# Optimization experiments

Measured on AMD Instinct MI355X. Metric: run time of the kernel, lower is better.

Reference implementation:

```python
import jax, jax.numpy as jnp
import numpy as np

N, D, K = 131072, 256, 16      # samples, ambient dim, projection dims
NDOM, B, G = 8, 32, 100        # domains, hist_bins, barycenter grid size


def setup_inputs() -> dict:
    key = jax.random.key(0)
    k1, k2, k3, k4, k5, k6 = jax.random.split(key, 6)
    X = jax.random.normal(k1, (N, D), jnp.float32)
    y = jax.random.randint(k2, (N,), 0, NDOM)
    # wT: orthonormal columns via QR with sign fix (as in INB.__init__)
    wi = np.asarray(jax.random.normal(k3, (D, K), jnp.float32))
    Q, R = np.linalg.qr(wi)
    wT = jnp.asarray(Q * np.sign(np.diag(R)), jnp.float32)
    # Per-(domain, dim) histogram bin edges (sorted -> monotone) and CDF values in [0,1]
    bin_edges = jnp.sort(jax.random.normal(k4, (NDOM, K, B + 1), jnp.float32) * 2.0, axis=-1)
    steps = jax.random.uniform(k5, (NDOM, K, B), jnp.float32, minval=0.1, maxval=1.0)
    c = jnp.cumsum(steps, axis=-1)
    cdf_vals = jnp.concatenate([jnp.zeros((NDOM, K, 1), jnp.float32), c / c[..., -1:]], axis=-1)
    # Barycenter inverse-CDF (quantile function) sampled on a uniform grid over [0,1]
    bary_q = jnp.sort(jax.random.normal(k6, (K, G), jnp.float32) * 2.0, axis=-1)
    return {"X": X, "y": y, "wT": wT, "bin_edges": bin_edges,
            "cdf_vals": cdf_vals, "bary_q": bary_q}


def _searchsorted_2d(edges, x):
    # edges: (N, K, B+1) per-sample monotone edges; x: (N, K)
    ss = jax.vmap(jax.vmap(lambda e, v: jnp.searchsorted(e, v, side='right')))(edges, x)
    return jnp.clip(ss - 1, 0, B - 1)  # (N, K) int, left bin index


def reference(X, y, wT, bin_edges, cdf_vals, bary_q):
    Xm = X @ wT                         # (N, K) small-K GEMM
    remaining = X - Xm @ wT.T           # (N, D)
    # gather per-sample domain tables (irregular, data-dependent access)
    eb = bin_edges[y]                   # (N, K, B+1)
    cb = cdf_vals[y]                    # (N, K, B+1)
    i = _searchsorted_2d(eb, Xm)        # (N, K)
    x0 = jnp.take_along_axis(eb, i[..., None], axis=-1)[..., 0]
    x1 = jnp.take_along_axis(eb, i[..., None] + 1, axis=-1)[..., 0]
    f0 = jnp.take_along_axis(cb, i[..., None], axis=-1)[..., 0]
    f1 = jnp.take_along_axis(cb, i[..., None] + 1, axis=-1)[..., 0]
    t = jnp.clip((Xm - x0) / (x1 - x0), 0.0, 1.0)
    u = f0 + t * (f1 - f0)              # per-domain CDF value in [0,1]
    # barycenter inverse CDF: linear interp on uniform grid over [0,1]
    pos = jnp.clip(u, 0.0, 1.0) * (G - 1)
    j = jnp.clip(pos.astype(jnp.int32), 0, G - 2)
    tt = pos - j.astype(pos.dtype)
    kk = jnp.arange(K)[None, :]
    z = bary_q[kk, j] * (1.0 - tt) + bary_q[kk, j + 1] * tt  # (N, K)
    return remaining + z @ wT.T
```

## Files before the change

### kernel.cpp

```cpp
#include <hip/hip_runtime.h>

typedef float v2f __attribute__((ext_vector_type(2)));
typedef float v4f __attribute__((ext_vector_type(4)));

#define N_ROWS 131072
#define DIM    256
#define KP     16
#define NDOM   8
#define NB     32
#define GG     100

#define EB_N   (NDOM*KP*(NB+1))
#define BARY_N (KP*GG)

#define GRID   2048
#define WAVES  4
#define NWAVE  (GRID*WAVES)
#define PAIRS  8

__device__ __forceinline__ v2f swap32_sum(v2f lo, v2f hi, int lane) {
    bool up = (lane & 32) != 0;
    v2f keep = up ? hi : lo;
    v2f send = up ? lo : hi;
    v2f r;
    r[0] = keep[0] + __shfl_xor(send[0], 32);
    r[1] = keep[1] + __shfl_xor(send[1], 32);
    return r;
}
__device__ __forceinline__ v2f swap16_sum(v2f lo, v2f hi, int lane) {
    bool up = (lane & 16) != 0;
    v2f keep = up ? hi : lo;
    v2f send = up ? lo : hi;
    v2f r;
    r[0] = keep[0] + __shfl_xor(send[0], 16);
    r[1] = keep[1] + __shfl_xor(send[1], 16);
    return r;
}
template <int CTRL>
__device__ __forceinline__ float dppf(float x) {
    return __builtin_bit_cast(float, __builtin_amdgcn_update_dpp(
        0, __builtin_bit_cast(int, x), CTRL, 0xF, 0xF, true));
}
template <int CTRL>
__device__ __forceinline__ int dppi(int x) {
    return __builtin_amdgcn_update_dpp(0, x, CTRL, 0xF, 0xF, true);
}
__device__ __forceinline__ float red16(float v) {
    v += dppf<0xB1>(v);
    v += dppf<0x4E>(v);
    v += dppf<0x141>(v);
    v += dppf<0x140>(v);
    return v;
}
__device__ __forceinline__ void wave_fence() {
    asm volatile("s_waitcnt lgkmcnt(0)" ::: "memory");
    __builtin_amdgcn_sched_barrier(0);
}

__device__ __forceinline__ void proj_row(v4f x, const v2f wTo[4][8], v2f P[8]) {
#pragma unroll
    for (int q = 0; q < 8; ++q) P[q] = (v2f){0.f, 0.f};
#pragma unroll
    for (int j = 0; j < 4; ++j) {
        v2f xj = {x[j], x[j]};
#pragma unroll
        for (int q = 0; q < 8; ++q) P[q] += xj * wTo[j][q];
    }
}

__device__ __forceinline__ float reduce_scatter(v2f P[8], int lane) {
    v2f Q[4];
#pragma unroll
    for (int r = 0; r < 4; ++r)
        Q[r] = swap32_sum(P[r], P[r+4], lane);
    v2f S0 = swap16_sum(Q[0], Q[2], lane);
    v2f S1 = swap16_sum(Q[1], Q[3], lane);
    float a = red16(S0[0]), b = red16(S0[1]);
    float c = red16(S1[0]), d = red16(S1[1]);
    float lo = (lane & 1) ? b : a;
    float hi = (lane & 1) ? d : c;
    return (lane & 2) ? hi : lo;
}

__device__ __forceinline__ float quantile_map(float xm, const float* ebRow,
                                              const float* cfRow, const float* bqk,
                                              const float e[8]) {
    int cnt = (e[0] <= xm) + (e[1] <= xm) + (e[2] <= xm) + (e[3] <= xm)
            + (e[4] <= xm) + (e[5] <= xm) + (e[6] <= xm) + (e[7] <= xm);
    cnt += dppi<0x124>(cnt);
    cnt += dppi<0x128>(cnt);
    int i0 = min(max(cnt - 1, 0), NB - 1);
    float x0 = ebRow[i0], x1 = ebRow[i0+1];
    float f0 = cfRow[i0], f1 = cfRow[i0+1];
    float t  = fminf(fmaxf(__fdividef(xm - x0, x1 - x0), 0.f), 1.f);
    float u  = f0 + t * (f1 - f0);
    float posv = fminf(fmaxf(u, 0.f), 1.f) * (float)(GG - 1);
    int jj = min((int)posv, GG - 2);
    float ttf = posv - (float)jj;
    float b0 = bqk[jj], b1 = bqk[jj+1];
    return xm - (b0*(1.f - ttf) + b1*ttf);
}

__device__ __forceinline__ void out_row(v4f x, const float* cb, const v2f wTo[4][8],
                                        float* op) {
    v2f c2[8];
#pragma unroll
    for (int q = 0; q < 4; ++q) {
        v4f cv4 = *reinterpret_cast<const v4f*>(&cb[4*q]);
        c2[2*q]   = (v2f){cv4[0], cv4[1]};
        c2[2*q+1] = (v2f){cv4[2], cv4[3]};
    }
    v4f o4;
#pragma unroll
    for (int j = 0; j < 4; ++j) {
        v2f a = c2[0] * wTo[j][0];
#pragma unroll
        for (int q = 1; q < 8; ++q) a += c2[q] * wTo[j][q];
        o4[j] = x[j] - (a[0] + a[1]);
    }
    *reinterpret_cast<v4f*>(op) = o4;
}

__global__ __launch_bounds__(256, 4)
void inb_kernel(const float* __restrict__ X, const int* __restrict__ y,
                const float* __restrict__ wT, const float* __restrict__ be,
                const float* __restrict__ cv, const float* __restrict__ bq,
                float* __restrict__ out)
{
    __shared__ alignas(16) float sEB[EB_N];
    __shared__ alignas(16) float sCOEFF[WAVES][32];

    const int tid = threadIdx.x;
    for (int i = tid; i < EB_N; i += 256) sEB[i] = be[i];
    __syncthreads();

    const int lane = tid & 63;
    const int wid  = tid >> 6;
    const int k  = ((lane & 48) >> 2) | (lane & 3);
    const int ec = (lane >> 2) & 3;

    v2f wTo[4][8];
#pragma unroll
    for (int j = 0; j < 4; ++j) {
        const v4f* wrow = reinterpret_cast<const v4f*>(&wT[(4*lane + j)*KP]);
#pragma unroll
        for (int q = 0; q < 4; ++q) {
            v4f v = wrow[q];
            wTo[j][2*q]   = (v2f){v[0], v[1]};
            wTo[j][2*q+1] = (v2f){v[2], v[3]};
        }
    }

    float* cobuf = sCOEFF[wid];
    const float* bqk = bq + k*GG;
    const int gwave = blockIdx.x * WAVES + wid;
    const int xoff  = 4*lane;

    v4f xA = *reinterpret_cast<const v4f*>(&X[(size_t)gwave*DIM + xoff]);
    v4f xB = *reinterpret_cast<const v4f*>(&X[(size_t)(gwave + NWAVE)*DIM + xoff]);
    int dA = y[gwave], dB = y[gwave + NWAVE];

    for (int it = 0; it < PAIRS; ++it) {
        const int rA = gwave + (2*it)*NWAVE;
        const int rB = rA + NWAVE;

        const float* ebA = &sEB[(dA*KP + k)*(NB+1)];
        const float* ebB = &sEB[(dB*KP + k)*(NB+1)];
        float eA[8], eB[8];
#pragma unroll
        for (int t = 0; t < 8; ++t) { eA[t] = ebA[8*ec + t]; eB[t] = ebB[8*ec + t]; }

        int nA = rA + 2*NWAVE; if (nA >= N_ROWS) nA = rA;
        int nB = nA + NWAVE;   if (nB >= N_ROWS) nB = rA;
        int dA_n = y[nA], dB_n = y[nB];
        v4f xA_n = *reinterpret_cast<const v4f*>(&X[(size_t)nA*DIM + xoff]);
        v4f xB_n = *reinterpret_cast<const v4f*>(&X[(size_t)nB*DIM + xoff]);

        v2f PA[8], PB[8];
        proj_row(xA, wTo, PA);
        proj_row(xB, wTo, PB);

        float xmA = reduce_scatter(PA, lane);
        float xmB = reduce_scatter(PB, lane);

        float cA = quantile_map(xmA, ebA, cv + (size_t)(dA*KP + k)*(NB+1), bqk, eA);
        float cB = quantile_map(xmB, ebB, cv + (size_t)(dB*KP + k)*(NB+1), bqk, eB);

        if (ec < 2) cobuf[ec*16 + k] = (ec == 0) ? cA : cB;
        wave_fence();

        out_row(xA, cobuf,      wTo, &out[(size_t)rA*DIM + xoff]);
        out_row(xB, cobuf + 16, wTo, &out[(size_t)rB*DIM + xoff]);

        xA = xA_n; xB = xB_n; dA = dA_n; dB = dB_n;
    }
}

extern "C" void kernel_launch(void* const* d_in, const int* in_sizes, int n_in,
                              void* d_out, int out_size, void* d_ws, size_t ws_size,
                              hipStream_t stream) {
    const float* X  = (const float*)d_in[0];
    const int*   y  = (const int*)  d_in[1];
    const float* wT = (const float*)d_in[2];
    const float* be = (const float*)d_in[3];
    const float* cv = (const float*)d_in[4];
    const float* bq = (const float*)d_in[5];
    float* out = (float*)d_out;
    hipLaunchKernelGGL(inb_kernel, dim3(GRID), dim3(256), 0, stream,
                       X, y, wT, be, cv, bq, out);
}
```

Measured before the change: 77.50 us.

## Software-pipeline quantile chain with output emission and stage tables in LDS

```diff
diff --git a/kernel.cpp b/kernel.cpp
--- a/kernel.cpp
+++ b/kernel.cpp
@@ -13,10 +13,10 @@
 #define EB_N   (NDOM*KP*(NB+1))
 #define BARY_N (KP*GG)
 
-#define GRID   2048
+#define GRID   1024
 #define WAVES  4
 #define NWAVE  (GRID*WAVES)
-#define PAIRS  8
+#define PAIRS  16
 
 __device__ __forceinline__ v2f swap32_sum(v2f lo, v2f hi, int lane) {
     bool up = (lane & 32) != 0;
@@ -55,17 +55,6 @@
 __device__ __forceinline__ void wave_fence() {
     asm volatile("s_waitcnt lgkmcnt(0)" ::: "memory");
     __builtin_amdgcn_sched_barrier(0);
-}
-
-__device__ __forceinline__ void proj_row(v4f x, const v2f wTo[4][8], v2f P[8]) {
-#pragma unroll
-    for (int q = 0; q < 8; ++q) P[q] = (v2f){0.f, 0.f};
-#pragma unroll
-    for (int j = 0; j < 4; ++j) {
-        v2f xj = {x[j], x[j]};
-#pragma unroll
-        for (int q = 0; q < 8; ++q) P[q] += xj * wTo[j][q];
-    }
 }
 
 __device__ __forceinline__ float reduce_scatter(v2f P[8], int lane) {
@@ -82,15 +71,32 @@
     return (lane & 2) ? hi : lo;
 }
 
-__device__ __forceinline__ float quantile_map(float xm, const float* ebRow,
-                                              const float* cfRow, const float* bqk,
-                                              const float e[8]) {
+__device__ __forceinline__ float chain_row(v4f x, int dom, const v2f wTo[4][8],
+                                           const float* sEB_, const float* sCDF_,
+                                           const float* bqk, int k, int ec, int lane) {
+    const float* ebRow = &sEB_[(dom*KP + k)*(NB+1)];
+    float e[8];
+#pragma unroll
+    for (int t = 0; t < 8; ++t) e[t] = ebRow[8*ec + t];
+
+    v2f P[8];
+#pragma unroll
+    for (int q = 0; q < 8; ++q) P[q] = (v2f){0.f, 0.f};
+#pragma unroll
+    for (int j = 0; j < 4; ++j) {
+        v2f xj = {x[j], x[j]};
+#pragma unroll
+        for (int q = 0; q < 8; ++q) P[q] += xj * wTo[j][q];
+    }
+    float xm = reduce_scatter(P, lane);
+
     int cnt = (e[0] <= xm) + (e[1] <= xm) + (e[2] <= xm) + (e[3] <= xm)
             + (e[4] <= xm) + (e[5] <= xm) + (e[6] <= xm) + (e[7] <= xm);
     cnt += dppi<0x124>(cnt);
     cnt += dppi<0x128>(cnt);
     int i0 = min(max(cnt - 1, 0), NB - 1);
     float x0 = ebRow[i0], x1 = ebRow[i0+1];
+    const float* cfRow = &sCDF_[(dom*KP + k)*(NB+1)];
     float f0 = cfRow[i0], f1 = cfRow[i0+1];
     float t  = fminf(fmaxf(__fdividef(xm - x0, x1 - x0), 0.f), 1.f);
     float u  = f0 + t * (f1 - f0);
@@ -101,15 +107,16 @@
     return xm - (b0*(1.f - ttf) + b1*ttf);
 }
 
-__device__ __forceinline__ void out_row(v4f x, const float* cb, const v2f wTo[4][8],
-                                        float* op) {
-    v2f c2[8];
+__device__ __forceinline__ void load_coeffs(const float* cb, v2f c2[8]) {
 #pragma unroll
     for (int q = 0; q < 4; ++q) {
         v4f cv4 = *reinterpret_cast<const v4f*>(&cb[4*q]);
         c2[2*q]   = (v2f){cv4[0], cv4[1]};
         c2[2*q+1] = (v2f){cv4[2], cv4[3]};
     }
+}
+__device__ __forceinline__ void emit_row(v4f x, const v2f c2[8], const v2f wTo[4][8],
+                                         float* op) {
     v4f o4;
 #pragma unroll
     for (int j = 0; j < 4; ++j) {
@@ -128,10 +135,13 @@
                 float* __restrict__ out)
 {
     __shared__ alignas(16) float sEB[EB_N];
+    __shared__ alignas(16) float sCDF[EB_N];
+    __shared__ alignas(16) float sBARY[BARY_N];
     __shared__ alignas(16) float sCOEFF[WAVES][32];
 
     const int tid = threadIdx.x;
-    for (int i = tid; i < EB_N; i += 256) sEB[i] = be[i];
+    for (int i = tid; i < EB_N; i += 256) { sEB[i] = be[i]; sCDF[i] = cv[i]; }
+    for (int i = tid; i < BARY_N; i += 256) sBARY[i] = bq[i];
     __syncthreads();
 
     const int lane = tid & 63;
@@ -152,48 +162,57 @@
     }
 
     float* cobuf = sCOEFF[wid];
-    const float* bqk = bq + k*GG;
+    const float* bqk = &sBARY[k*GG];
     const int gwave = blockIdx.x * WAVES + wid;
     const int xoff  = 4*lane;
 
-    v4f xA = *reinterpret_cast<const v4f*>(&X[(size_t)gwave*DIM + xoff]);
-    v4f xB = *reinterpret_cast<const v4f*>(&X[(size_t)(gwave + NWAVE)*DIM + xoff]);
-    int dA = y[gwave], dB = y[gwave + NWAVE];
-
-    for (int it = 0; it < PAIRS; ++it) {
+    v4f xA_c = *reinterpret_cast<const v4f*>(&X[(size_t)gwave*DIM + xoff]);
+    v4f xB_c = *reinterpret_cast<const v4f*>(&X[(size_t)(gwave + NWAVE)*DIM + xoff]);
+    int dA_c = y[gwave], dB_c = y[gwave + NWAVE];
+    v4f xA_n = *reinterpret_cast<const v4f*>(&X[(size_t)(gwave + 2*NWAVE)*DIM + xoff]);
+    v4f xB_n = *reinterpret_cast<const v4f*>(&X[(size_t)(gwave + 3*NWAVE)*DIM + xoff]);
+    int dA_n = y[gwave + 2*NWAVE], dB_n = y[gwave + 3*NWAVE];
+
+    {
+        float cA = chain_row(xA_c, dA_c, wTo, sEB, sCDF, bqk, k, ec, lane);
+        float cB = chain_row(xB_c, dB_c, wTo, sEB, sCDF, bqk, k, ec, lane);
+        if (ec < 2) cobuf[ec*16 + k] = (ec == 0) ? cA : cB;
+    }
+    v4f xA_o = xA_c, xB_o = xB_c;
+    int r_o = gwave;
+    xA_c = xA_n; xB_c = xB_n; dA_c = dA_n; dB_c = dB_n;
+
+    for (int it = 1; it < PAIRS; ++it) {
         const int rA = gwave + (2*it)*NWAVE;
-        const int rB = rA + NWAVE;
-
-        const float* ebA = &sEB[(dA*KP + k)*(NB+1)];
-        const float* ebB = &sEB[(dB*KP + k)*(NB+1)];
-        float eA[8], eB[8];
-#pragma unroll
-        for (int t = 0; t < 8; ++t) { eA[t] = ebA[8*ec + t]; eB[t] = ebB[8*ec + t]; }
-
-        int nA = rA + 2*NWAVE; if (nA >= N_ROWS) nA = rA;
-        int nB = nA + NWAVE;   if (nB >= N_ROWS) nB = rA;
-        int dA_n = y[nA], dB_n = y[nB];
-        v4f xA_n = *reinterpret_cast<const v4f*>(&X[(size_t)nA*DIM + xoff]);
-        v4f xB_n = *reinterpret_cast<const v4f*>(&X[(size_t)nB*DIM + xoff]);
-
-        v2f PA[8], PB[8];
-        proj_row(xA, wTo, PA);
-        proj_row(xB, wTo, PB);
-
-        float xmA = reduce_scatter(PA, lane);
-        float xmB = reduce_scatter(PB, lane);
-
-        float cA = quantile_map(xmA, ebA, cv + (size_t)(dA*KP + k)*(NB+1), bqk, eA);
-        float cB = quantile_map(xmB, ebB, cv + (size_t)(dB*KP + k)*(NB+1), bqk, eB);
-
+
+        wave_fence();
+
+        v2f c2A[8], c2B[8];
+        load_coeffs(cobuf,      c2A);
+        load_coeffs(cobuf + 16, c2B);
+
+        int pfA = (it + 1 < PAIRS) ? rA + 2*NWAVE : rA;
+        v4f xA_p = *reinterpret_cast<const v4f*>(&X[(size_t)pfA*DIM + xoff]);
+        v4f xB_p = *reinterpret_cast<const v4f*>(&X[(size_t)(pfA + NWAVE)*DIM + xoff]);
+        int dA_p = y[pfA], dB_p = y[pfA + NWAVE];
+
+        float cA = chain_row(xA_c, dA_c, wTo, sEB, sCDF, bqk, k, ec, lane);
+        float cB = chain_row(xB_c, dB_c, wTo, sEB, sCDF, bqk, k, ec, lane);
         if (ec < 2) cobuf[ec*16 + k] = (ec == 0) ? cA : cB;
-        wave_fence();
-
-        out_row(xA, cobuf,      wTo, &out[(size_t)rA*DIM + xoff]);
-        out_row(xB, cobuf + 16, wTo, &out[(size_t)rB*DIM + xoff]);
-
-        xA = xA_n; xB = xB_n; dA = dA_n; dB = dB_n;
-    }
+
+        emit_row(xA_o, c2A, wTo, &out[(size_t)r_o*DIM + xoff]);
+        emit_row(xB_o, c2B, wTo, &out[(size_t)(r_o + NWAVE)*DIM + xoff]);
+
+        xA_o = xA_c; xB_o = xB_c; r_o = rA;
+        xA_c = xA_p; xB_c = xB_p; dA_c = dA_p; dB_c = dB_p;
+    }
+
+    wave_fence();
+    v2f c2A[8], c2B[8];
+    load_coeffs(cobuf,      c2A);
+    load_coeffs(cobuf + 16, c2B);
+    emit_row(xA_o, c2A, wTo, &out[(size_t)r_o*DIM + xoff]);
+    emit_row(xB_o, c2B, wTo, &out[(size_t)(r_o + NWAVE)*DIM + xoff]);
 }
 
 extern "C" void kernel_launch(void* const* d_in, const int* in_sizes, int n_in,
```

Result: slower. 214.1 us (+176.2%).
